# Kernel optimization log

Hardware: AMD Instinct MI355X
Metric: run time of the kernel (lower is better)

## Reference

```python
import jax, jax.numpy as jnp
import numpy as np

N_REC = 12288  # 12 * nside^2, nside=32


def _mlp(x, w1, b1, w2, b2):
    # two-layer MLP with SiLU, as in GraphCast-style edge embedders
    return jnp.dot(jax.nn.silu(jnp.dot(x, w1) + b1), w2) + b2


def setup_inputs() -> dict:
    key = jax.random.key(0)
    ks = jax.random.split(key, 12)
    B, E, D_X, D_EDGE = 2, 393216, 128, 4
    EDGE_IN, EDGE_OUT, LIN_OUT = D_EDGE + D_X, 256, 256

    def glorot(k, shape):
        fan = shape[0] + shape[1]
        return jax.random.normal(k, shape, jnp.float32) * jnp.sqrt(2.0 / fan)

    return {
        "x": jax.random.normal(ks[0], (B, E, D_X), jnp.float32),
        "edge_attr": jax.random.normal(ks[1], (E, D_EDGE), jnp.float32),
        "edge_index": jax.random.randint(ks[2], (2, E), 0, N_REC, jnp.int64),
        "w1e": glorot(ks[3], (EDGE_IN, EDGE_OUT)),
        "b1e": jnp.zeros((EDGE_OUT,), jnp.float32),
        "w2e": glorot(ks[4], (EDGE_OUT, EDGE_OUT)),
        "b2e": jnp.zeros((EDGE_OUT,), jnp.float32),
        "w1f": glorot(ks[5], (EDGE_OUT, LIN_OUT)),
        "b1f": jnp.zeros((LIN_OUT,), jnp.float32),
        "w2f": glorot(ks[6], (LIN_OUT, LIN_OUT)),
        "b2f": jnp.zeros((LIN_OUT,), jnp.float32),
    }


def reference(x, edge_attr, edge_index, w1e, b1e, w2e, b2e, w1f, b1f, w2f, b2f):
    B = x.shape[0]
    # broadcast edge_attr over batch and concat with per-edge grid features
    ea = jnp.broadcast_to(edge_attr[None], (B,) + edge_attr.shape)  # [B,E,d_edge]
    v_g_prime = jnp.concatenate([ea, x], axis=-1)                    # [B,E,edge_in]
    v_g = _mlp(v_g_prime, w1e, b1e, w2e, b2e)                        # [B,E,edge_out]
    # scatter-sum edges into receiver nodes (edge_index[1]) along dim 1
    recv = edge_index[1]
    v_m_sum = jnp.zeros((B, N_REC, v_g.shape[-1]), v_g.dtype).at[:, recv].add(v_g)
    return _mlp(v_m_sum, w1f, b1f, w2f, b2f)                         # [B,N_REC,lin_out]
```

## Files before the change

kernel.cpp:

```cpp
#include <hip/hip_runtime.h>
#include <hip/hip_bf16.h>

#define E_EDGES 393216
#define NRECV   12288
#define DX      128
#define BATCH   2

typedef short bf16x8 __attribute__((ext_vector_type(8)));
typedef float f32x4  __attribute__((ext_vector_type(4)));

__device__ __forceinline__ unsigned short f2bf(float f) {
  union { float f; unsigned u; } v; v.f = f;
  unsigned r = v.u + 0x7FFFu + ((v.u >> 16) & 1u);
  return (unsigned short)(r >> 16);
}

__device__ __forceinline__ unsigned pk2(float a, float b) {
  __hip_bfloat162 h = __float22bfloat162_rn(make_float2(a, b));
  union { __hip_bfloat162 h; unsigned u; } c; c.h = h;
  return c.u;
}

__device__ __forceinline__ float silu_f(float v) {
  return v / (1.0f + __expf(-v));
}

__global__ __launch_bounds__(256) void zero_kernel(float4* __restrict__ p, int n4) {
  int i = blockIdx.x * 256 + threadIdx.x;
  int stride = gridDim.x * 256;
  float4 z = make_float4(0.f, 0.f, 0.f, 0.f);
  for (; i < n4; i += stride) p[i] = z;
}

__global__ void swz_kernel(const float* __restrict__ W,
                           unsigned short* __restrict__ out, int K, int N) {
  int t = blockIdx.x * 256 + threadIdx.x;
  if (t >= K * N) return;
  int j = t & 7;
  int l = (t >> 3) & 63;
  int rest = t >> 9;
  int nfr = N >> 4;
  int nf = rest % nfr;
  int ks = rest / nfr;
  int k = ks * 32 + (l >> 4) * 8 + j;
  int n = nf * 16 + (l & 15);
  out[t] = f2bf(W[k * N + n]);
}

__global__ void swz_w1e_kernel(const float* __restrict__ W,
                               unsigned short* __restrict__ out) {
  int t = blockIdx.x * 256 + threadIdx.x;
  int j = t & 7;
  int l = (t >> 3) & 63;
  int rest = t >> 9;
  int nf = rest & 15;
  int ks = rest >> 4;
  int k = ks * 32 + (l >> 4) * 8 + j;
  int n = nf * 16 + (l & 15);
  out[t] = (k < 132) ? f2bf(W[k * 256 + n]) : (unsigned short)0;
}

__global__ void hist_kernel(const int* __restrict__ recv, int* __restrict__ cnt) {
  int e = blockIdx.x * 256 + threadIdx.x;
  if (e < E_EDGES) atomicAdd(&cnt[recv[e]], 1);
}

__global__ __launch_bounds__(256) void scan_kernel(const int* __restrict__ cnt,
                                                   int* __restrict__ head) {
  __shared__ int ts[256];
  const int t = threadIdx.x;
  const int base = t * 48;
  int s = 0;
#pragma unroll
  for (int i = 0; i < 48; ++i) s += cnt[base + i];
  ts[t] = s;
  __syncthreads();
  for (int d = 1; d < 256; d <<= 1) {
    int v = (t >= d) ? ts[t - d] : 0;
    __syncthreads();
    ts[t] += v;
    __syncthreads();
  }
  int run = (t == 0) ? 0 : ts[t - 1];
  for (int i = 0; i < 48; ++i) { head[base + i] = run; run += cnt[base + i]; }
}

__global__ void scatter_kernel(const int* __restrict__ recv, int* __restrict__ head,
                               int* __restrict__ perm) {
  int e = blockIdx.x * 256 + threadIdx.x;
  if (e < E_EDGES) {
    int pos = atomicAdd(&head[recv[e]], 1);
    perm[pos] = e;
  }
}

__global__ __launch_bounds__(256, 4) void edge_kernel(
    const float* __restrict__ x, const float* __restrict__ edge_attr,
    const int* __restrict__ recv, const int* __restrict__ perm,
    const float* __restrict__ b1e, const unsigned short* __restrict__ w1sw,
    float* __restrict__ s) {
  __shared__ unsigned short hs[64 * 264];
  __shared__ float b1lds[256];
  __shared__ int ev[64];
  __shared__ int rs[64];
  char* As = (char*)hs;

  const int tid = threadIdx.x;
  const int l  = tid & 63;
  const int w  = tid >> 6;
  const int lo = l & 15, hi = l >> 4;
  const int p0 = blockIdx.x * 64;
  const int b  = blockIdx.y;

  if (tid < 64) {
    int e = perm[p0 + tid];
    ev[tid] = e;
    rs[tid] = recv[e];
  }
  b1lds[tid] = b1e[tid];
  for (int idx = tid; idx < 960; idx += 256) {
    int r = idx / 15, k2 = idx - r * 15;
    int byte0 = 264 + 8 * k2;
    *(uint2*)(As + r * 384 + (byte0 ^ ((r & 7) << 4))) = make_uint2(0u, 0u);
  }
  __syncthreads();

  {
    const int r = tid >> 2, q = tid & 3;
    const int e = ev[r];
    const int rx = (r & 7) << 4;
    const float4* xr = (const float4*)(x + ((size_t)b * E_EDGES + e) * DX);
#pragma unroll
    for (int i = 0; i < 8; ++i) {
      int t = q * 8 + i;
      float4 v = xr[t];
      int byte0 = 8 + 8 * t;
      *(uint2*)(As + r * 384 + (byte0 ^ rx)) = make_uint2(pk2(v.x, v.y), pk2(v.z, v.w));
    }
    if (tid < 64) {
      float4 ea = *(const float4*)(edge_attr + (size_t)ev[tid] * 4);
      *(uint2*)(As + tid * 384 + ((tid & 7) << 4)) =
          make_uint2(pk2(ea.x, ea.y), pk2(ea.z, ea.w));
    }
  }
  __syncthreads();

  f32x4 acc[4][4] = {};
  const int axor = (lo & 7) << 4;
#pragma unroll
  for (int kk = 0; kk < 5; ++kk) {
    bf16x8 a[4], bb[4];
#pragma unroll
    for (int mf = 0; mf < 4; ++mf)
      a[mf] = *(const bf16x8*)(As + (mf * 16 + lo) * 384 + ((kk * 64 + hi * 16) ^ axor));
#pragma unroll
    for (int nf = 0; nf < 4; ++nf)
      bb[nf] = *(const bf16x8*)&w1sw[(size_t)(((kk * 16) + (w * 4 + nf)) * 64 + l) * 8];
#pragma unroll
    for (int mf = 0; mf < 4; ++mf)
#pragma unroll
      for (int nf = 0; nf < 4; ++nf)
        acc[mf][nf] = __builtin_amdgcn_mfma_f32_16x16x32_bf16(a[mf], bb[nf], acc[mf][nf], 0, 0, 0);
  }
  __syncthreads();

#pragma unroll
  for (int mf = 0; mf < 4; ++mf) {
#pragma unroll
    for (int nf = 0; nf < 4; ++nf) {
      const int col = w * 64 + nf * 16 + lo;
      const float bb1 = b1lds[col];
#pragma unroll
      for (int j = 0; j < 4; ++j) {
        const int row = mf * 16 + hi * 4 + j;
        hs[row * 264 + col] = f2bf(silu_f(acc[mf][nf][j] + bb1));
      }
    }
  }
  __syncthreads();

  {
    int flag = (l == 63) || (rs[l + 1] != rs[l]);
    unsigned long long segmask = __ballot(flag);
    float* sb = s + (size_t)b * NRECV * 256 + tid;
    float run = 0.0f;
#pragma unroll
    for (int r = 0; r < 64; ++r) {
      union { unsigned u; float f; } c;
      c.u = (unsigned)hs[r * 264 + tid] << 16;
      run += c.f;
      if ((segmask >> r) & 1ull) {
        atomicAdd(sb + (size_t)rs[r] * 256, run);
        run = 0.0f;
      }
    }
  }
}

__device__ __forceinline__ void gemm64(const unsigned short* Ns,
                                       const unsigned short* __restrict__ Bsw,
                                       int w, int l, f32x4 acc[4][4]) {
  const int lo = l & 15, hi = l >> 4;
#pragma unroll
  for (int kk = 0; kk < 8; ++kk) {
    bf16x8 a[4], bb[4];
#pragma unroll
    for (int mf = 0; mf < 4; ++mf)
      a[mf] = *(const bf16x8*)&Ns[(mf * 16 + lo) * 264 + kk * 32 + hi * 8];
#pragma unroll
    for (int nf = 0; nf < 4; ++nf)
      bb[nf] = *(const bf16x8*)&Bsw[(size_t)(((kk * 16) + (w * 4 + nf)) * 64 + l) * 8];
#pragma unroll
    for (int mf = 0; mf < 4; ++mf)
#pragma unroll
      for (int nf = 0; nf < 4; ++nf)
        acc[mf][nf] = __builtin_amdgcn_mfma_f32_16x16x32_bf16(a[mf], bb[nf], acc[mf][nf], 0, 0, 0);
  }
}

__global__ __launch_bounds__(256) void node_kernel(
    const float* __restrict__ s, const int* __restrict__ cnt,
    const unsigned short* __restrict__ w2esw, const float* __restrict__ b2e,
    const unsigned short* __restrict__ w1fsw, const float* __restrict__ b1f,
    const unsigned short* __restrict__ w2fsw, const float* __restrict__ b2f,
    float* __restrict__ out) {
  __shared__ unsigned short Ns[64 * 264];
  __shared__ int   cntl[64];
  __shared__ float bias1[256], bias2[256], bias3[256];

  const int tid = threadIdx.x;
  const int l  = tid & 63;
  const int w  = tid >> 6;
  const int lo = l & 15, hi = l >> 4;
  const int r0 = blockIdx.x * 64;
  const int b  = blockIdx.y;

  const float4* sb = (const float4*)(s + ((size_t)b * NRECV + r0) * 256);
#pragma unroll
  for (int i = 0; i < 16; ++i) {
    int f = i * 256 + tid;
    float4 v = sb[f];
    int g = f * 4;
    int row = g >> 8, col = g & 255;
    *(uint2*)&Ns[row * 264 + col] = make_uint2(pk2(v.x, v.y), pk2(v.z, v.w));
  }
  if (tid < 64) cntl[tid] = cnt[r0 + tid];
  bias1[tid] = b2e[tid];
  bias2[tid] = b1f[tid];
  bias3[tid] = b2f[tid];
  __syncthreads();

  {
    f32x4 acc[4][4] = {};
    gemm64(Ns, w2esw, w, l, acc);
    __syncthreads();
#pragma unroll
    for (int mf = 0; mf < 4; ++mf)
#pragma unroll
      for (int nf = 0; nf < 4; ++nf) {
        const int col = w * 64 + nf * 16 + lo;
#pragma unroll
        for (int j = 0; j < 4; ++j) {
          const int row = mf * 16 + hi * 4 + j;
          float v = acc[mf][nf][j] + (float)cntl[row] * bias1[col];
          Ns[row * 264 + col] = f2bf(v);
        }
      }
    __syncthreads();
  }
  {
    f32x4 acc[4][4] = {};
    gemm64(Ns, w1fsw, w, l, acc);
    __syncthreads();
#pragma unroll
    for (int mf = 0; mf < 4; ++mf)
#pragma unroll
      for (int nf = 0; nf < 4; ++nf) {
        const int col = w * 64 + nf * 16 + lo;
#pragma unroll
        for (int j = 0; j < 4; ++j) {
          const int row = mf * 16 + hi * 4 + j;
          float v = silu_f(acc[mf][nf][j] + bias2[col]);
          Ns[row * 264 + col] = f2bf(v);
        }
      }
    __syncthreads();
  }
  {
    f32x4 acc[4][4] = {};
    gemm64(Ns, w2fsw, w, l, acc);
#pragma unroll
    for (int mf = 0; mf < 4; ++mf)
#pragma unroll
      for (int nf = 0; nf < 4; ++nf) {
        const int col = w * 64 + nf * 16 + lo;
#pragma unroll
        for (int j = 0; j < 4; ++j) {
          const int row = mf * 16 + hi * 4 + j;
          out[((size_t)b * NRECV + r0 + row) * 256 + col] = acc[mf][nf][j] + bias3[col];
        }
      }
  }
}

extern "C" void kernel_launch(void* const* d_in, const int* in_sizes, int n_in,
                              void* d_out, int out_size, void* d_ws, size_t ws_size,
                              hipStream_t stream) {
  const float* x         = (const float*)d_in[0];
  const float* edge_attr = (const float*)d_in[1];
  const int*   edge_idx  = (const int*)d_in[2];
  const float* w1e       = (const float*)d_in[3];
  const float* b1e       = (const float*)d_in[4];
  const float* w2e       = (const float*)d_in[5];
  const float* b2e       = (const float*)d_in[6];
  const float* w1f       = (const float*)d_in[7];
  const float* b1f       = (const float*)d_in[8];
  const float* w2f       = (const float*)d_in[9];
  const float* b2f       = (const float*)d_in[10];
  float* out = (float*)d_out;

  char* ws = (char*)d_ws;
  float*          sbuf  = (float*)(ws + 0);
  int*            cnt   = (int*)(ws + 25165824);
  int*            head  = (int*)(ws + 25214976);
  int*            perm  = (int*)(ws + 25264128);
  unsigned short* w1sw  = (unsigned short*)(ws + 26836992);
  unsigned short* w2esw = (unsigned short*)(ws + 26918912);
  unsigned short* w1fsw = (unsigned short*)(ws + 27049984);
  unsigned short* w2fsw = (unsigned short*)(ws + 27181056);

  zero_kernel<<<2048, 256, 0, stream>>>((float4*)ws, 1575936);

  swz_w1e_kernel<<<160, 256, 0, stream>>>(w1e, w1sw);
  swz_kernel<<<(256 * 256) / 256, 256, 0, stream>>>(w2e, w2esw, 256, 256);
  swz_kernel<<<(256 * 256) / 256, 256, 0, stream>>>(w1f, w1fsw, 256, 256);
  swz_kernel<<<(256 * 256) / 256, 256, 0, stream>>>(w2f, w2fsw, 256, 256);

  const int* recv = edge_idx + E_EDGES;
  hist_kernel<<<E_EDGES / 256, 256, 0, stream>>>(recv, cnt);
  scan_kernel<<<1, 256, 0, stream>>>(cnt, head);
  scatter_kernel<<<E_EDGES / 256, 256, 0, stream>>>(recv, head, perm);

  dim3 eg(E_EDGES / 64, BATCH);
  edge_kernel<<<eg, 256, 0, stream>>>(x, edge_attr, recv, perm, b1e, w1sw, sbuf);

  dim3 ng(NRECV / 64, BATCH);
  node_kernel<<<ng, 256, 0, stream>>>(sbuf, cnt, w2esw, b2e, w1fsw, b1f, w2fsw, b2f, out);
}
```

Before: 293.6 us.

## Segment-sum edge features via indicator-matrix MFMA and fold bias into GEMM

```diff
diff --git a/kernel.cpp b/kernel.cpp
--- a/kernel.cpp
+++ b/kernel.cpp
@@ -47,7 +47,7 @@
   out[t] = f2bf(W[k * N + n]);
 }
 
-__global__ void swz_w1e_kernel(const float* __restrict__ W,
+__global__ void swz_w1e_kernel(const float* __restrict__ W, const float* __restrict__ bias,
                                unsigned short* __restrict__ out) {
   int t = blockIdx.x * 256 + threadIdx.x;
   int j = t & 7;
@@ -57,7 +57,8 @@
   int ks = rest >> 4;
   int k = ks * 32 + (l >> 4) * 8 + j;
   int n = nf * 16 + (l & 15);
-  out[t] = (k < 132) ? f2bf(W[k * 256 + n]) : (unsigned short)0;
+  float v = (k < 132) ? W[k * 256 + n] : (k == 132 ? bias[n] : 0.0f);
+  out[t] = f2bf(v);
 }
 
 __global__ void hist_kernel(const int* __restrict__ recv, int* __restrict__ cnt) {
@@ -97,13 +98,14 @@
 __global__ __launch_bounds__(256, 4) void edge_kernel(
     const float* __restrict__ x, const float* __restrict__ edge_attr,
     const int* __restrict__ recv, const int* __restrict__ perm,
-    const float* __restrict__ b1e, const unsigned short* __restrict__ w1sw,
-    float* __restrict__ s) {
-  __shared__ unsigned short hs[64 * 264];
-  __shared__ float b1lds[256];
+    const unsigned short* __restrict__ w1sw, float* __restrict__ s) {
+  __shared__ __align__(16) char hsT[256 * 144];
+  __shared__ __align__(16) char indT[16 * 144];
+  __shared__ unsigned int seg32[16];
+  __shared__ int seg_recv[64];
   __shared__ int ev[64];
   __shared__ int rs[64];
-  char* As = (char*)hs;
+  char* As = hsT;
 
   const int tid = threadIdx.x;
   const int l  = tid & 63;
@@ -117,11 +119,11 @@
     ev[tid] = e;
     rs[tid] = recv[e];
   }
-  b1lds[tid] = b1e[tid];
   for (int idx = tid; idx < 960; idx += 256) {
     int r = idx / 15, k2 = idx - r * 15;
     int byte0 = 264 + 8 * k2;
-    *(uint2*)(As + r * 384 + (byte0 ^ ((r & 7) << 4))) = make_uint2(0u, 0u);
+    uint2 vz = make_uint2(k2 == 0 ? 0x00003F80u : 0u, 0u);
+    *(uint2*)(As + r * 384 + (byte0 ^ ((r & 7) << 4))) = vz;
   }
   __syncthreads();
 
@@ -132,18 +134,35 @@
     const float4* xr = (const float4*)(x + ((size_t)b * E_EDGES + e) * DX);
 #pragma unroll
     for (int i = 0; i < 8; ++i) {
-      int t = q * 8 + i;
+      int t = i * 4 + q;
       float4 v = xr[t];
       int byte0 = 8 + 8 * t;
       *(uint2*)(As + r * 384 + (byte0 ^ rx)) = make_uint2(pk2(v.x, v.y), pk2(v.z, v.w));
     }
-    if (tid < 64) {
-      float4 ea = *(const float4*)(edge_attr + (size_t)ev[tid] * 4);
-      *(uint2*)(As + tid * 384 + ((tid & 7) << 4)) =
-          make_uint2(pk2(ea.x, ea.y), pk2(ea.z, ea.w));
-    }
-  }
-  __syncthreads();
+  }
+  const int flag = (l == 63) || (rs[l + 1] != rs[l]);
+  const unsigned long long segmask = __ballot(flag);
+  const int nseg = __popcll(segmask);
+  if (tid < 64) {
+    float4 ea = *(const float4*)(edge_attr + (size_t)ev[tid] * 4);
+    *(uint2*)(As + tid * 384 + ((tid & 7) << 4)) =
+        make_uint2(pk2(ea.x, ea.y), pk2(ea.z, ea.w));
+    int sid = __popcll(segmask & ((1ull << tid) - 1ull));
+    ((unsigned char*)seg32)[tid] = (unsigned char)sid;
+    if (flag) seg_recv[sid] = rs[tid];
+  }
+  __syncthreads();
+
+  {
+    int m = tid & 15, k4 = tid >> 4;
+    unsigned four = seg32[k4];
+    unsigned um = (unsigned)m;
+    unsigned e0 = ((four & 255u) == um) ? 0x3F80u : 0u;
+    unsigned e1 = (((four >> 8) & 255u) == um) ? 0x3F80u : 0u;
+    unsigned e2 = (((four >> 16) & 255u) == um) ? 0x3F80u : 0u;
+    unsigned e3 = ((four >> 24) == um) ? 0x3F80u : 0u;
+    *(uint2*)(indT + m * 144 + k4 * 8) = make_uint2(e0 | (e1 << 16), e2 | (e3 << 16));
+  }
 
   f32x4 acc[4][4] = {};
   const int axor = (lo & 7) << 4;
@@ -169,31 +188,52 @@
 #pragma unroll
     for (int nf = 0; nf < 4; ++nf) {
       const int col = w * 64 + nf * 16 + lo;
-      const float bb1 = b1lds[col];
-#pragma unroll
-      for (int j = 0; j < 4; ++j) {
-        const int row = mf * 16 + hi * 4 + j;
-        hs[row * 264 + col] = f2bf(silu_f(acc[mf][nf][j] + bb1));
-      }
-    }
-  }
-  __syncthreads();
-
-  {
-    int flag = (l == 63) || (rs[l + 1] != rs[l]);
-    unsigned long long segmask = __ballot(flag);
-    float* sb = s + (size_t)b * NRECV * 256 + tid;
-    float run = 0.0f;
-#pragma unroll
-    for (int r = 0; r < 64; ++r) {
-      union { unsigned u; float f; } c;
-      c.u = (unsigned)hs[r * 264 + tid] << 16;
-      run += c.f;
-      if ((segmask >> r) & 1ull) {
-        atomicAdd(sb + (size_t)rs[r] * 256, run);
-        run = 0.0f;
-      }
-    }
+      float v0 = silu_f(acc[mf][nf][0]);
+      float v1 = silu_f(acc[mf][nf][1]);
+      float v2 = silu_f(acc[mf][nf][2]);
+      float v3 = silu_f(acc[mf][nf][3]);
+      *(uint2*)(hsT + col * 144 + (mf * 16 + hi * 4) * 2) =
+          make_uint2(pk2(v0, v1), pk2(v2, v3));
+    }
+  }
+  __syncthreads();
+
+  float* sb = s + (size_t)b * NRECV * 256;
+  for (int p = 0;;) {
+    f32x4 accS[4] = {};
+#pragma unroll
+    for (int kk = 0; kk < 2; ++kk) {
+      bf16x8 a = *(const bf16x8*)(indT + lo * 144 + kk * 64 + hi * 16);
+#pragma unroll
+      for (int nf = 0; nf < 4; ++nf) {
+        bf16x8 bb = *(const bf16x8*)(hsT + (w * 64 + nf * 16 + lo) * 144 + kk * 64 + hi * 16);
+        accS[nf] = __builtin_amdgcn_mfma_f32_16x16x32_bf16(a, bb, accS[nf], 0, 0, 0);
+      }
+    }
+#pragma unroll
+    for (int j = 0; j < 4; ++j) {
+      int sidx = p * 16 + hi * 4 + j;
+      if (sidx < nseg) {
+        int rcv = seg_recv[sidx];
+#pragma unroll
+        for (int nf = 0; nf < 4; ++nf)
+          atomicAdd(sb + (size_t)rcv * 256 + w * 64 + nf * 16 + lo, accS[nf][j]);
+      }
+    }
+    ++p;
+    if (p * 16 >= nseg) break;
+    __syncthreads();
+    {
+      int m = tid & 15, k4 = tid >> 4;
+      unsigned four = seg32[k4];
+      unsigned um = (unsigned)(m + p * 16);
+      unsigned e0 = ((four & 255u) == um) ? 0x3F80u : 0u;
+      unsigned e1 = (((four >> 8) & 255u) == um) ? 0x3F80u : 0u;
+      unsigned e2 = (((four >> 16) & 255u) == um) ? 0x3F80u : 0u;
+      unsigned e3 = ((four >> 24) == um) ? 0x3F80u : 0u;
+      *(uint2*)(indT + m * 144 + k4 * 8) = make_uint2(e0 | (e1 << 16), e2 | (e3 << 16));
+    }
+    __syncthreads();
   }
 }
 
@@ -331,7 +371,7 @@
 
   zero_kernel<<<2048, 256, 0, stream>>>((float4*)ws, 1575936);
 
-  swz_w1e_kernel<<<160, 256, 0, stream>>>(w1e, w1sw);
+  swz_w1e_kernel<<<160, 256, 0, stream>>>(w1e, b1e, w1sw);
   swz_kernel<<<(256 * 256) / 256, 256, 0, stream>>>(w2e, w2esw, 256, 256);
   swz_kernel<<<(256 * 256) / 256, 256, 0, stream>>>(w1f, w1fsw, 256, 256);
   swz_kernel<<<(256 * 256) / 256, 256, 0, stream>>>(w2f, w2fsw, 256, 256);
@@ -342,7 +382,7 @@
   scatter_kernel<<<E_EDGES / 256, 256, 0, stream>>>(recv, head, perm);
 
   dim3 eg(E_EDGES / 64, BATCH);
-  edge_kernel<<<eg, 256, 0, stream>>>(x, edge_attr, recv, perm, b1e, w1sw, sbuf);
+  edge_kernel<<<eg, 256, 0, stream>>>(x, edge_attr, recv, perm, w1sw, sbuf);
 
   dim3 ng(NRECV / 64, BATCH);
   node_kernel<<<ng, 256, 0, stream>>>(sbuf, cnt, w2esw, b2e, w1fsw, b1f, w2fsw, b2f, out);
```

New measurement: 278.6 us. 5.1% less time.
